# Optimization experiments

Hardware: AMD Instinct MI355X
Metric: run time of the kernel (lower is better)

Reference implementation:

```python
import jax, jax.numpy as jnp
import numpy as np

H = 8        # heads
DH = 64      # dim_head
K = 16       # num_neighbors
EMB = 512    # emb_dim
INNER = H * DH
AINNER = 4 * DH  # per-head attn_mlp hidden width
POSH = 64


def setup_inputs() -> dict:
    key = jax.random.key(0)
    ks = jax.random.split(key, 20)
    bs, n = 2, 1024
    rn = lambda k, s, sc=1.0: jax.random.normal(k, s, jnp.float32) * sc
    return {
        "query": rn(ks[0], (bs, n, EMB)),
        "key_in": rn(ks[1], (bs, n, EMB)),
        "value": rn(ks[2], (bs, n, EMB)),
        "canonical": rn(ks[3], (bs, n, 3)),
        "w_q": rn(ks[4], (EMB, INNER), EMB ** -0.5),
        "w_k": rn(ks[5], (EMB, INNER), EMB ** -0.5),
        "w_v": rn(ks[6], (EMB, INNER), EMB ** -0.5),
        "w_out": rn(ks[7], (INNER, EMB), INNER ** -0.5),
        "b_out": rn(ks[8], (EMB,), 0.02),
        "pos_w1": rn(ks[9], (3, POSH), 3 ** -0.5),
        "pos_b1": rn(ks[10], (POSH,), 0.02),
        "pos_w2": rn(ks[11], (POSH, INNER), POSH ** -0.5),
        "pos_b2": rn(ks[12], (INNER,), 0.02),
        "aw1": rn(ks[13], (H, AINNER, DH), DH ** -0.5),   # grouped conv1 weight per head: (out=4*DH, in=DH)
        "ab1": rn(ks[14], (H, AINNER), 0.02),
        "aw2": rn(ks[15], (H, DH, AINNER), AINNER ** -0.5),  # grouped conv2: (out=DH, in=4*DH)
        "ab2": rn(ks[16], (H, DH), 0.02),
    }


def reference(query, key_in, value, canonical, w_q, w_k, w_v, w_out, b_out,
              pos_w1, pos_b1, pos_w2, pos_b2, aw1, ab1, aw2, ab2):
    bs, n, _ = query.shape
    # projections, then b n (h d) -> b h n d
    to_heads = lambda t: t.reshape(bs, n, H, DH).transpose(0, 2, 1, 3)
    q = to_heads(query @ w_q)
    k = to_heads(key_in @ w_k)
    v = to_heads(value @ w_v)

    # KNN on canonical coords: (b,n,n) squared distances, k smallest (includes self)
    d2 = jnp.sum((canonical[:, :, None, :] - canonical[:, None, :, :]) ** 2, axis=-1)
    _, nbr = jax.lax.top_k(-d2, K)                       # (b,n,K)
    idx = (nbr + (jnp.arange(bs) * n)[:, None, None]).reshape(-1)  # flat rows into bs*n

    # relative position embedding
    pos_nn = canonical.reshape(bs * n, 3)[idx].reshape(bs, n, K, 3)
    rel = pos_nn - canonical[:, :, None, :]
    rpe = jax.nn.relu(rel @ pos_w1 + pos_b1) @ pos_w2 + pos_b2        # (b,n,K,inner)
    rpe = rpe.reshape(bs, n, K, H, DH).transpose(0, 3, 1, 2, 4)       # (b,h,i,j,d)

    # faithful replication of the original view(bs*n,-1)[idx] gathers on (b,h,n,d) tensors
    gather = lambda t: t.reshape(bs * n, -1)[idx].reshape(bs, H, n, K, DH)
    qg, kg, vg = gather(q), gather(k), gather(v)
    vg = vg + rpe
    x = (qg - kg) + rpe                                  # (b,h,i,j,d)

    # grouped 1x1 conv attn_mlp == per-head MLP over d
    hdn = jax.nn.relu(jnp.einsum('bhijd,hed->bhije', x, aw1) + ab1[None, :, None, None, :])
    sim = jnp.einsum('bhije,hde->bhijd', hdn, aw2) + ab2[None, :, None, None, :]

    attn = jax.nn.softmax(sim, axis=3)                   # softmax over neighbors j
    norm = jnp.sqrt(jnp.sum(attn * attn, axis=2, keepdims=True))  # F.normalize over i
    attn = attn / jnp.maximum(norm, 1e-12)

    agg = jnp.einsum('bhijd,bhijd->bhid', attn, vg)      # (b,h,i,d)
    agg = agg.transpose(0, 2, 1, 3).reshape(bs, n, INNER)
    return agg @ w_out + b_out
```

## Files before the change

kernel.cpp:

```cpp
#include <hip/hip_runtime.h>


#define BS 2
#define NPT 1024
#define HH 8
#define DH 64
#define KNN 16
#define EMB 512
#define INNER 512
#define AINNER 256
#define POSH 64

typedef unsigned short u16;
typedef unsigned int u32;
typedef __attribute__((ext_vector_type(8))) short bf16x8;
typedef __attribute__((ext_vector_type(4))) float f32x4;

__device__ __forceinline__ float bf2f(u16 b) { union { u32 u; float f; } v; v.u = ((u32)b) << 16; return v.f; }
__device__ __forceinline__ u16 f2bf_rne(float f) {
    u32 x = __float_as_uint(f);
    u32 r = x + 0x7fffu + ((x >> 16) & 1u);
    return (u16)(r >> 16);
}
__device__ __forceinline__ void split2(float f, u16& hi, u16& lo) {
    u32 bits = __float_as_uint(f);
    hi = (u16)(bits >> 16);
    float resid = f - __uint_as_float(bits & 0xffff0000u);
    lo = (u16)(__float_as_uint(resid) >> 16);
}
__device__ __forceinline__ void split4(float4 f, ushort4& h, ushort4& l) {
    split2(f.x, h.x, l.x); split2(f.y, h.y, l.y);
    split2(f.z, h.z, l.z); split2(f.w, h.w, l.w);
}

__global__ __launch_bounds__(256) void k_preT(const float* __restrict__ aw1,
                                              const float* __restrict__ aw2,
                                              const float* __restrict__ pw2,
                                              const float* __restrict__ wq,
                                              const float* __restrict__ wk,
                                              const float* __restrict__ wv,
                                              const float* __restrict__ wout,
                                              u16* __restrict__ w1hi, u16* __restrict__ w2hi,
                                              u16* __restrict__ rw2hi,
                                              u16* __restrict__ o0h, u16* __restrict__ o0l,
                                              u16* __restrict__ o1h, u16* __restrict__ o1l,
                                              u16* __restrict__ o2h, u16* __restrict__ o2l,
                                              u16* __restrict__ o3h, u16* __restrict__ o3l)
{
    __shared__ float S[64][65];
    const int bx = blockIdx.x, t = threadIdx.x;
    if (bx < 1152) {
        int idx = bx * 256 + t;
        if (idx < 131072) {
            w1hi[idx] = f2bf_rne(aw1[idx]);
        } else if (idx < 262144) {
            int k2 = idx - 131072;
            w2hi[k2] = f2bf_rne(aw2[k2]);
        } else {
            int k2 = idx - 262144;
            int p = k2 & 63; int hd = k2 >> 6;
            int h = hd >> 6; int d = hd & 63;
            rw2hi[k2] = f2bf_rne(pw2[(size_t)p * INNER + h * DH + d]);
        }
        return;
    }
    const int v0 = bx - 1152;
    const int e0 = (v0 & 7) * 64, c0 = ((v0 >> 3) & 7) * 64, z = v0 >> 6;
    const float* src; u16* dh; u16* dl;
    switch (z) {
        case 0:  src = wq;   dh = o0h; dl = o0l; break;
        case 1:  src = wk;   dh = o1h; dl = o1l; break;
        case 2:  src = wv;   dh = o2h; dl = o2l; break;
        default: src = wout; dh = o3h; dl = o3l; break;
    }
    #pragma unroll
    for (int s = 0; s < 16; ++s) {
        int v = s * 256 + t; int r = v >> 6, c = v & 63;
        S[r][c] = src[(size_t)(e0 + r) * 512 + c0 + c];
    }
    __syncthreads();
    #pragma unroll
    for (int s = 0; s < 16; ++s) {
        int v = s * 256 + t; int c = v >> 6, e = v & 63;
        u16 hi, lo; split2(S[e][c], hi, lo);
        size_t off = (size_t)(c0 + c) * 512 + e0 + e;
        dh[off] = hi; dl[off] = lo;
    }
}

__global__ __launch_bounds__(256) void k_projM(const float* __restrict__ qf,
                                               const float* __restrict__ kf,
                                               const float* __restrict__ vf,
                                               const u16* __restrict__ wqh, const u16* __restrict__ wql,
                                               const u16* __restrict__ wkh, const u16* __restrict__ wkl,
                                               const u16* __restrict__ wvh, const u16* __restrict__ wvl,
                                               float* __restrict__ Dws, float* __restrict__ Vws)
{
    __shared__ u16 S[12][64 * 40];
    const int t = threadIdx.x, l = t & 63, w = t >> 6;
    const int lm = l & 15, lg = (l >> 4) * 8;
    const int g0 = blockIdx.x * 64, c0 = blockIdx.y * 64;
    const int sr = t >> 2, sc = (t & 3) * 8;

    f32x4 accD[4] = {{0,0,0,0},{0,0,0,0},{0,0,0,0},{0,0,0,0}};
    f32x4 accV[4] = {{0,0,0,0},{0,0,0,0},{0,0,0,0},{0,0,0,0}};

    for (int ks = 0; ks < 16; ++ks) {
        const int k0 = ks * 32;
        if (ks) __syncthreads();
        #pragma unroll
        for (int m = 0; m < 3; ++m) {
            const float* sp = (m == 0 ? qf : (m == 1 ? kf : vf))
                              + (size_t)(g0 + sr) * 512 + k0 + sc;
            float4 f0 = *(const float4*)sp;
            float4 f1 = *(const float4*)(sp + 4);
            if (m == 1) {
                f0.x = -f0.x; f0.y = -f0.y; f0.z = -f0.z; f0.w = -f0.w;
                f1.x = -f1.x; f1.y = -f1.y; f1.z = -f1.z; f1.w = -f1.w;
            }
            ushort4 h0, l0, h1, l1;
            split4(f0, h0, l0); split4(f1, h1, l1);
            *(ushort4*)&S[2*m  ][sr * 40 + sc]     = h0;
            *(ushort4*)&S[2*m  ][sr * 40 + sc + 4] = h1;
            *(ushort4*)&S[2*m+1][sr * 40 + sc]     = l0;
            *(ushort4*)&S[2*m+1][sr * 40 + sc + 4] = l1;
        }
        #define STG(p, base) \
            *(uint4*)&S[p][sr * 40 + sc] = *(const uint4*)&(base)[(size_t)(c0 + sr) * 512 + k0 + sc];
        STG(6, wqh) STG(7, wql) STG(8, wkh) STG(9, wkl) STG(10, wvh) STG(11, wvl)
        #undef STG
        __syncthreads();

        const int ao = (w * 16 + lm) * 40 + lg;
        bf16x8 aqh = *(const bf16x8*)&S[0][ao];
        bf16x8 aql = *(const bf16x8*)&S[1][ao];
        bf16x8 akh = *(const bf16x8*)&S[2][ao];
        bf16x8 akl = *(const bf16x8*)&S[3][ao];
        bf16x8 avh = *(const bf16x8*)&S[4][ao];
        bf16x8 avl = *(const bf16x8*)&S[5][ao];
        #pragma unroll
        for (int ct = 0; ct < 4; ++ct) {
            const int bo = (ct * 16 + lm) * 40 + lg;
            bf16x8 bqh = *(const bf16x8*)&S[6][bo];
            bf16x8 bql = *(const bf16x8*)&S[7][bo];
            bf16x8 bkh = *(const bf16x8*)&S[8][bo];
            bf16x8 bkl = *(const bf16x8*)&S[9][bo];
            bf16x8 bvh = *(const bf16x8*)&S[10][bo];
            bf16x8 bvl = *(const bf16x8*)&S[11][bo];
            accD[ct] = __builtin_amdgcn_mfma_f32_16x16x32_bf16(aqh, bqh, accD[ct], 0, 0, 0);
            accD[ct] = __builtin_amdgcn_mfma_f32_16x16x32_bf16(aql, bqh, accD[ct], 0, 0, 0);
            accD[ct] = __builtin_amdgcn_mfma_f32_16x16x32_bf16(aqh, bql, accD[ct], 0, 0, 0);
            accD[ct] = __builtin_amdgcn_mfma_f32_16x16x32_bf16(akh, bkh, accD[ct], 0, 0, 0);
            accD[ct] = __builtin_amdgcn_mfma_f32_16x16x32_bf16(akl, bkh, accD[ct], 0, 0, 0);
            accD[ct] = __builtin_amdgcn_mfma_f32_16x16x32_bf16(akh, bkl, accD[ct], 0, 0, 0);
            accV[ct] = __builtin_amdgcn_mfma_f32_16x16x32_bf16(avh, bvh, accV[ct], 0, 0, 0);
            accV[ct] = __builtin_amdgcn_mfma_f32_16x16x32_bf16(avl, bvh, accV[ct], 0, 0, 0);
            accV[ct] = __builtin_amdgcn_mfma_f32_16x16x32_bf16(avh, bvl, accV[ct], 0, 0, 0);
        }
    }

    const int b = blockIdx.x >> 4;
    const int h = blockIdx.y;
    #pragma unroll
    for (int ct = 0; ct < 4; ++ct) {
        #pragma unroll
        for (int r = 0; r < 4; ++r) {
            int g = g0 + w * 16 + (l >> 4) * 4 + r;
            int i = g & 1023;
            size_t off = (((size_t)(b * HH + h)) * NPT + i) * DH + ct * 16 + lm;
            Dws[off] = accD[ct][r];
            Vws[off] = accV[ct][r];
        }
    }
}

__global__ __launch_bounds__(256) void k_knn(const float* __restrict__ canonical,
                                             const float* __restrict__ pw1,
                                             const float* __restrict__ pb1,
                                             int* __restrict__ nbr,
                                             u16* __restrict__ h1g)
{
    const int t = threadIdx.x, l = t & 63, w = t >> 6;
    const int i = blockIdx.x * 4 + w;
    const int b = blockIdx.y;
    const float* cb = canonical + (size_t)b * NPT * 3;
    const float qx = cb[i*3+0], qy = cb[i*3+1], qz = cb[i*3+2];
    float d2v[16];
    #pragma unroll
    for (int k = 0; k < 16; ++k) {
        int j = l * 16 + k;
        float dx = __fsub_rn(cb[j*3+0], qx);
        float dy = __fsub_rn(cb[j*3+1], qy);
        float dz = __fsub_rn(cb[j*3+2], qz);
        d2v[k] = __fadd_rn(__fadd_rn(__fmul_rn(dx,dx), __fmul_rn(dy,dy)), __fmul_rn(dz,dz));
    }
    unsigned alive = 0xFFFFu;
    int js[16];
    int* out = nbr + ((size_t)b * NPT + i) * KNN;
    #pragma unroll
    for (int sel = 0; sel < KNN; ++sel) {
        float bv = __builtin_inff(); int bk = 16;
        #pragma unroll
        for (int k = 0; k < 16; ++k) {
            float v = ((alive >> k) & 1u) ? d2v[k] : __builtin_inff();
            if (v < bv) { bv = v; bk = k; }
        }
        int bj = l * 16 + bk;
        #pragma unroll
        for (int m = 32; m >= 1; m >>= 1) {
            float ov = __shfl_xor(bv, m, 64);
            int   oj = __shfl_xor(bj, m, 64);
            if (ov < bv || (ov == bv && oj < bj)) { bv = ov; bj = oj; }
        }
        if (l == 0) out[sel] = bj;
        js[sel] = bj;
        if ((bj >> 4) == l) alive &= ~(1u << (bj & 15));
    }
    const float pw10 = pw1[l], pw11 = pw1[64 + l], pw12 = pw1[128 + l], pb1v = pb1[l];
    u16* hrow = h1g + (((size_t)b * NPT + i) * KNN) * 64 + l;
    #pragma unroll
    for (int j = 0; j < KNN; ++j) {
        int nv = js[j];
        float rx = cb[nv*3+0] - qx;
        float ry = cb[nv*3+1] - qy;
        float rz = cb[nv*3+2] - qz;
        float a = pb1v;
        a = fmaf(rx, pw10, a);
        a = fmaf(ry, pw11, a);
        a = fmaf(rz, pw12, a);
        hrow[j * 64] = f2bf_rne(fmaxf(a, 0.0f));
    }
}

__global__ __launch_bounds__(256, 3) void k_attn(const float* __restrict__ Dws,
                                              const float* __restrict__ Vws,
                                              const int* __restrict__ nbr,
                                              const float* __restrict__ pb2,
                                              const float* __restrict__ ab1,
                                              const float* __restrict__ ab2,
                                              const u16* __restrict__ w1hi,
                                              const u16* __restrict__ w2hi,
                                              const u16* __restrict__ rw2hi,
                                              const u16* __restrict__ h1g,
                                              u16* __restrict__ vvb,
                                              u16* __restrict__ attnb,
                                              float* __restrict__ npart2)
{
    const int it = blockIdx.x, h = blockIdx.y, b = blockIdx.z, t = threadIdx.x;
    const int l = t & 63, w = t >> 6;
    const int lm = l & 15, lg = (l >> 4) * 8;
    const int dd = w * 16 + lm;

    __shared__ u16 Xs[2][16 * 72];
    __shared__ u16 Hs[2][16 * 264];
    __shared__ u16 rw2s[64 * 72];
    __shared__ int nbrrow[KNN];

    bf16x8 w1f[8], w2f[8];
    float b1v[4];
    #pragma unroll
    for (int q = 0; q < 4; ++q) {
        int e = (w * 4 + q) * 16 + lm;
        b1v[q] = ab1[h * AINNER + e];
        #pragma unroll
        for (int kc = 0; kc < 2; ++kc)
            w1f[q*2+kc] = *(const bf16x8*)&w1hi[((size_t)(h * AINNER + e)) * DH + kc * 32 + lg];
    }
    const float b2v  = ab2[h * DH + dd];
    const float pb2v = pb2[h * DH + dd];
    #pragma unroll
    for (int kc = 0; kc < 8; ++kc)
        w2f[kc] = *(const bf16x8*)&w2hi[((size_t)(h * DH + dd)) * AINNER + kc * 32 + lg];

    for (int v = t; v < 64 * 64; v += 256) {
        int d = v >> 6, p = v & 63;
        rw2s[d * 72 + p] = rw2hi[(h * DH + d) * POSH + p];
    }
    if (t < KNN) nbrrow[t] = nbr[((size_t)b * NPT + h * 128 + it) * KNN + t];
    __syncthreads();

    float dvp[2][4], vwp[2][4];
    bf16x8 h1f[2][2];
    auto gather = [&](int pp) {
        #pragma unroll
        for (int u = 0; u < 2; ++u) {
            const int ti = 2 * pp + u;
            const int i = it * 8 + ti;
            #pragma unroll
            for (int r = 0; r < 4; ++r) {
                int j = (l >> 4) * 4 + r;
                int nv = nbrrow[2 * ti + (j >> 3)];
                size_t off = (((size_t)b * HH + (nv >> 7)) * NPT + (nv & 127) * 8 + (j & 7)) * DH + dd;
                dvp[u][r] = Dws[off];
                vwp[u][r] = Vws[off];
            }
            const u16* hb = h1g + (((size_t)b * NPT + i) * KNN + lm) * 64;
            h1f[u][0] = *(const bf16x8*)&hb[lg];
            h1f[u][1] = *(const bf16x8*)&hb[32 + lg];
        }
    };
    gather(0);

    float npacc[4] = {0.f, 0.f, 0.f, 0.f};

    for (int p = 0; p < 4; ++p) {
        #pragma unroll
        for (int u = 0; u < 2; ++u) {
            const int i = it * 8 + 2 * p + u;
            f32x4 racc = {0.f, 0.f, 0.f, 0.f};
            #pragma unroll
            for (int kc = 0; kc < 2; ++kc) {
                bf16x8 rb = *(const bf16x8*)&rw2s[dd * 72 + kc * 32 + lg];
                racc = __builtin_amdgcn_mfma_f32_16x16x32_bf16(h1f[u][kc], rb, racc, 0, 0, 0);
            }
            u16* vvrow = vvb + (((size_t)(b * HH + h) * NPT + i) * KNN) * DH + dd;
            #pragma unroll
            for (int r = 0; r < 4; ++r) {
                int j = (l >> 4) * 4 + r;
                float rp = racc[r] + pb2v;
                Xs[u][j * 72 + dd] = f2bf_rne(dvp[u][r] + rp);
                vvrow[j * DH] = f2bf_rne(vwp[u][r] + rp);
            }
        }
        if (p < 3) gather(p + 1);
        __syncthreads();
        #pragma unroll
        for (int u = 0; u < 2; ++u) {
            f32x4 acc1[4] = {{0,0,0,0},{0,0,0,0},{0,0,0,0},{0,0,0,0}};
            #pragma unroll
            for (int kc = 0; kc < 2; ++kc) {
                bf16x8 ah = *(const bf16x8*)&Xs[u][lm * 72 + kc * 32 + lg];
                #pragma unroll
                for (int q = 0; q < 4; ++q)
                    acc1[q] = __builtin_amdgcn_mfma_f32_16x16x32_bf16(ah, w1f[q*2+kc], acc1[q], 0, 0, 0);
            }
            #pragma unroll
            for (int q = 0; q < 4; ++q) {
                int ee = (w * 4 + q) * 16 + lm;
                #pragma unroll
                for (int r = 0; r < 4; ++r) {
                    int jj = (l >> 4) * 4 + r;
                    Hs[u][jj * 264 + ee] = f2bf_rne(fmaxf(acc1[q][r] + b1v[q], 0.0f));
                }
            }
        }
        __syncthreads();
        #pragma unroll
        for (int u = 0; u < 2; ++u) {
            const int i = it * 8 + 2 * p + u;
            f32x4 acc2[4] = {{0,0,0,0},{0,0,0,0},{0,0,0,0},{0,0,0,0}};
            #pragma unroll
            for (int kc = 0; kc < 8; ++kc) {
                bf16x8 ah = *(const bf16x8*)&Hs[u][lm * 264 + kc * 32 + lg];
                acc2[kc & 3] = __builtin_amdgcn_mfma_f32_16x16x32_bf16(ah, w2f[kc], acc2[kc & 3], 0, 0, 0);
            }
            float sim[4];
            #pragma unroll
            for (int r = 0; r < 4; ++r)
                sim[r] = ((acc2[0][r] + acc2[1][r]) + (acc2[2][r] + acc2[3][r])) + b2v;
            float m = fmaxf(fmaxf(sim[0], sim[1]), fmaxf(sim[2], sim[3]));
            m = fmaxf(m, __shfl_xor(m, 16, 64));
            m = fmaxf(m, __shfl_xor(m, 32, 64));
            float ex[4], s = 0.0f;
            #pragma unroll
            for (int r = 0; r < 4; ++r) { ex[r] = __expf(sim[r] - m); s += ex[r]; }
            s += __shfl_xor(s, 16, 64);
            s += __shfl_xor(s, 32, 64);
            float inv = 1.0f / s;
            u16* ao = attnb + (((size_t)(b * HH + h) * NPT + i) * KNN) * DH + dd;
            #pragma unroll
            for (int r = 0; r < 4; ++r) {
                u16 abf16 = f2bf_rne(ex[r] * inv);
                ao[((l >> 4) * 4 + r) * DH] = abf16;
                float abf = bf2f(abf16);
                npacc[r] = fmaf(abf, abf, npacc[r]);
            }
        }
    }

    float* np = npart2 + ((size_t)((b * HH + h) * 128 + it)) * 1024 + ((l >> 4) * 4) * 64 + dd;
    #pragma unroll
    for (int r = 0; r < 4; ++r) np[r * 64] = npacc[r];
}

__global__ __launch_bounds__(256) void k_normR(const float* __restrict__ npart2, float* __restrict__ nrm)
{
    __shared__ float red[256];
    const int vout = blockIdx.x * 64 + (threadIdx.x & 63);
    const int chunk = threadIdx.x >> 6;
    const int bh = vout >> 10, jd = vout & 1023;
    const float* src = npart2 + (size_t)bh * 131072 + jd + (size_t)chunk * 32768;
    float s = 0.0f;
    #pragma unroll 4
    for (int k = 0; k < 32; ++k) s += src[k * 1024];
    red[threadIdx.x] = s;
    __syncthreads();
    if (chunk == 0) {
        float tot = (red[threadIdx.x] + red[threadIdx.x + 64])
                  + (red[threadIdx.x + 128] + red[threadIdx.x + 192]);
        nrm[vout] = sqrtf(tot);
    }
}

__global__ __launch_bounds__(256) void k_agg(const u16* __restrict__ attnb,
                                             const float* __restrict__ nrm,
                                             const u16* __restrict__ vvb,
                                             u16* __restrict__ agghi,
                                             u16* __restrict__ agglo)
{
    const int it = blockIdx.x, h = blockIdx.y, b = blockIdx.z, t = threadIdx.x;
    const int l = t & 63, w = t >> 6;
    const int i = it * 4 + w;
    __shared__ float rn[KNN * DH];
    for (int v = t; v < KNN * DH; v += 256)
        rn[v] = 1.0f / fmaxf(nrm[(size_t)(b * HH + h) * 1024 + v], 1e-12f);
    __syncthreads();
    const size_t row = ((size_t)(b * HH + h) * NPT + i) * (KNN * DH);
    bf16x8 a0 = *(const bf16x8*)&attnb[row + l * 8];
    bf16x8 a1 = *(const bf16x8*)&attnb[row + 512 + l * 8];
    bf16x8 q0 = *(const bf16x8*)&vvb[row + l * 8];
    bf16x8 q1 = *(const bf16x8*)&vvb[row + 512 + l * 8];
    const int dbase = (l & 7) * 8;
    float4 ra = *(const float4*)&rn[(l >> 3) * 64 + dbase];
    float4 rb = *(const float4*)&rn[(l >> 3) * 64 + dbase + 4];
    float4 rc = *(const float4*)&rn[(8 + (l >> 3)) * 64 + dbase];
    float4 rd = *(const float4*)&rn[(8 + (l >> 3)) * 64 + dbase + 4];
    const float r0[8] = {ra.x, ra.y, ra.z, ra.w, rb.x, rb.y, rb.z, rb.w};
    const float r1[8] = {rc.x, rc.y, rc.z, rc.w, rd.x, rd.y, rd.z, rd.w};
    float acc[8];
    #pragma unroll
    for (int e = 0; e < 8; ++e)
        acc[e] = bf2f((u16)a0[e]) * r0[e] * bf2f((u16)q0[e])
               + bf2f((u16)a1[e]) * r1[e] * bf2f((u16)q1[e]);
    #pragma unroll
    for (int mask = 8; mask <= 32; mask <<= 1)
        #pragma unroll
        for (int e = 0; e < 8; ++e)
            acc[e] += __shfl_xor(acc[e], mask, 64);
    if (l < 8) {
        size_t off = ((size_t)b * NPT + i) * INNER + h * DH + l * 8;
        ushort4 h0, l0, h1, l1;
        split2(acc[0], h0.x, l0.x); split2(acc[1], h0.y, l0.y);
        split2(acc[2], h0.z, l0.z); split2(acc[3], h0.w, l0.w);
        split2(acc[4], h1.x, l1.x); split2(acc[5], h1.y, l1.y);
        split2(acc[6], h1.z, l1.z); split2(acc[7], h1.w, l1.w);
        *(ushort4*)&agghi[off]     = h0;
        *(ushort4*)&agghi[off + 4] = h1;
        *(ushort4*)&agglo[off]     = l0;
        *(ushort4*)&agglo[off + 4] = l1;
    }
}

__global__ __launch_bounds__(256) void k_outM(const u16* __restrict__ agghi, const u16* __restrict__ agglo,
                                              const u16* __restrict__ wth, const u16* __restrict__ wtl,
                                              const float* __restrict__ bout,
                                              float* __restrict__ outp)
{
    __shared__ u16 S[4][64 * 40];
    const int t = threadIdx.x, l = t & 63, w = t >> 6;
    const int lm = l & 15, lg = (l >> 4) * 8;
    const int g0 = blockIdx.x * 64, c0 = blockIdx.y * 64;
    const int sr = t >> 2, sc = (t & 3) * 8;

    f32x4 acc[4] = {{0,0,0,0},{0,0,0,0},{0,0,0,0},{0,0,0,0}};
    float bv4[4];
    #pragma unroll
    for (int ct = 0; ct < 4; ++ct) bv4[ct] = bout[c0 + ct * 16 + lm];

    for (int ks = 0; ks < 16; ++ks) {
        const int k0 = ks * 32;
        if (ks) __syncthreads();
        *(uint4*)&S[0][sr * 40 + sc] = *(const uint4*)&agghi[(size_t)(g0 + sr) * 512 + k0 + sc];
        *(uint4*)&S[1][sr * 40 + sc] = *(const uint4*)&agglo[(size_t)(g0 + sr) * 512 + k0 + sc];
        *(uint4*)&S[2][sr * 40 + sc] = *(const uint4*)&wth[(size_t)(c0 + sr) * 512 + k0 + sc];
        *(uint4*)&S[3][sr * 40 + sc] = *(const uint4*)&wtl[(size_t)(c0 + sr) * 512 + k0 + sc];
        __syncthreads();

        const int ao = (w * 16 + lm) * 40 + lg;
        bf16x8 ah = *(const bf16x8*)&S[0][ao];
        bf16x8 al = *(const bf16x8*)&S[1][ao];
        #pragma unroll
        for (int ct = 0; ct < 4; ++ct) {
            const int bo = (ct * 16 + lm) * 40 + lg;
            bf16x8 bh = *(const bf16x8*)&S[2][bo];
            bf16x8 bl = *(const bf16x8*)&S[3][bo];
            acc[ct] = __builtin_amdgcn_mfma_f32_16x16x32_bf16(ah, bh, acc[ct], 0, 0, 0);
            acc[ct] = __builtin_amdgcn_mfma_f32_16x16x32_bf16(al, bh, acc[ct], 0, 0, 0);
            acc[ct] = __builtin_amdgcn_mfma_f32_16x16x32_bf16(ah, bl, acc[ct], 0, 0, 0);
        }
    }
    #pragma unroll
    for (int ct = 0; ct < 4; ++ct) {
        #pragma unroll
        for (int r = 0; r < 4; ++r) {
            int g = g0 + w * 16 + (l >> 4) * 4 + r;
            outp[(size_t)g * 512 + c0 + ct * 16 + lm] = acc[ct][r] + bv4[ct];
        }
    }
}

extern "C" void kernel_launch(void* const* d_in, const int* in_sizes, int n_in,
                              void* d_out, int out_size, void* d_ws, size_t ws_size,
                              hipStream_t stream) {
    const float* query     = (const float*)d_in[0];
    const float* key_in    = (const float*)d_in[1];
    const float* value     = (const float*)d_in[2];
    const float* canonical = (const float*)d_in[3];
    const float* wq   = (const float*)d_in[4];
    const float* wk   = (const float*)d_in[5];
    const float* wv   = (const float*)d_in[6];
    const float* wout = (const float*)d_in[7];
    const float* bout = (const float*)d_in[8];
    const float* pw1  = (const float*)d_in[9];
    const float* pb1  = (const float*)d_in[10];
    const float* pw2  = (const float*)d_in[11];
    const float* pb2  = (const float*)d_in[12];
    const float* aw1  = (const float*)d_in[13];
    const float* ab1  = (const float*)d_in[14];
    const float* aw2  = (const float*)d_in[15];
    const float* ab2  = (const float*)d_in[16];

    float* ws    = (float*)d_ws;
    float* Dws   = ws;
    float* Vws   = ws + 1048576;
    float* aggp  = ws + 2097152;
    float* nrm   = ws + 3162112;
    int*   nbr   = (int*)(ws + 3293184);
    float* attnR = ws + 3325952;

    u16* agghi = (u16*)aggp;
    u16* agglo = agghi + 1048576;

    u16* attnb = (u16*)attnR;
    u16* pl   = (u16*)(attnR + 8388608);
    u16* wqTh = pl;                u16* wqTl = pl + 262144;
    u16* wkTh = pl + 524288;       u16* wkTl = pl + 786432;
    u16* wvTh = pl + 1048576;      u16* wvTl = pl + 1310720;
    float* npart2 = attnR + 12582912;
    u16* h1g = (u16*)(attnR + 14680064);

    u16* u16b  = (u16*)(ws + 20103168);
    u16* w1hi  = u16b;
    u16* w2hi  = u16b + 262144;
    u16* rw2hi = u16b + 524288;
    u16* vvb   = u16b + 589824;
    u16* wouTh = u16b + 17367040;
    u16* wouTl = u16b + 17629184;

    k_preT<<<1408, 256, 0, stream>>>(aw1, aw2, pw2, wq, wk, wv, wout,
                                     w1hi, w2hi, rw2hi,
                                     wqTh, wqTl, wkTh, wkTl, wvTh, wvTl, wouTh, wouTl);
    k_knn<<<dim3(256, BS), 256, 0, stream>>>(canonical, pw1, pb1, nbr, h1g);
    k_projM<<<dim3(32, 8), 256, 0, stream>>>(query, key_in, value,
                                             wqTh, wqTl, wkTh, wkTl, wvTh, wvTl, Dws, Vws);
    k_attn<<<dim3(128, HH, BS), 256, 0, stream>>>(Dws, Vws, nbr, pb2, ab1, ab2,
                                                  w1hi, w2hi, rw2hi, h1g, vvb, attnb, npart2);
    k_normR<<<256, 256, 0, stream>>>(npart2, nrm);
    k_agg<<<dim3(256, HH, BS), 256, 0, stream>>>(attnb, nrm, vvb, agghi, agglo);
    k_outM<<<dim3(32, 8), 256, 0, stream>>>(agghi, agglo, wouTh, wouTl, bout, (float*)d_out);
}
```

Measured before the change: 148.4 us.

## Fuse attn*value product into attention kernel and register-prefetch GEMM tiles

The attention kernel now multiplies the softmax weights by the value-plus-position term in registers and writes a single bf16 product buffer, instead of writing separate attention and value buffers. The aggregation kernel then reads only that one buffer and scales it by the per-(i,d) inverse norm, which halves the large intermediate traffic. The two projection GEMM kernels also prefetch the next K-slice into registers while the current tile is computed, to hide global load latency. This costs extra registers, which may lower occupancy, and it changes rounding because the product is rounded to bf16 once rather than each factor separately.

Measured after the change: 169.7 us. 14.4% more time.

```diff
diff --git a/kernel.cpp b/kernel.cpp
--- a/kernel.cpp
+++ b/kernel.cpp
@@ -105,15 +105,31 @@
     f32x4 accD[4] = {{0,0,0,0},{0,0,0,0},{0,0,0,0},{0,0,0,0}};
     f32x4 accV[4] = {{0,0,0,0},{0,0,0,0},{0,0,0,0},{0,0,0,0}};
 
-    for (int ks = 0; ks < 16; ++ks) {
+    float4 fA[3][2];
+    uint4  wB[6];
+    auto ldregs = [&](int ks) {
         const int k0 = ks * 32;
-        if (ks) __syncthreads();
         #pragma unroll
         for (int m = 0; m < 3; ++m) {
             const float* sp = (m == 0 ? qf : (m == 1 ? kf : vf))
                               + (size_t)(g0 + sr) * 512 + k0 + sc;
-            float4 f0 = *(const float4*)sp;
-            float4 f1 = *(const float4*)(sp + 4);
+            fA[m][0] = *(const float4*)sp;
+            fA[m][1] = *(const float4*)(sp + 4);
+        }
+        wB[0] = *(const uint4*)&wqh[(size_t)(c0 + sr) * 512 + k0 + sc];
+        wB[1] = *(const uint4*)&wql[(size_t)(c0 + sr) * 512 + k0 + sc];
+        wB[2] = *(const uint4*)&wkh[(size_t)(c0 + sr) * 512 + k0 + sc];
+        wB[3] = *(const uint4*)&wkl[(size_t)(c0 + sr) * 512 + k0 + sc];
+        wB[4] = *(const uint4*)&wvh[(size_t)(c0 + sr) * 512 + k0 + sc];
+        wB[5] = *(const uint4*)&wvl[(size_t)(c0 + sr) * 512 + k0 + sc];
+    };
+    ldregs(0);
+
+    for (int ks = 0; ks < 16; ++ks) {
+        if (ks) __syncthreads();
+        #pragma unroll
+        for (int m = 0; m < 3; ++m) {
+            float4 f0 = fA[m][0], f1 = fA[m][1];
             if (m == 1) {
                 f0.x = -f0.x; f0.y = -f0.y; f0.z = -f0.z; f0.w = -f0.w;
                 f1.x = -f1.x; f1.y = -f1.y; f1.z = -f1.z; f1.w = -f1.w;
@@ -125,11 +141,11 @@
             *(ushort4*)&S[2*m+1][sr * 40 + sc]     = l0;
             *(ushort4*)&S[2*m+1][sr * 40 + sc + 4] = l1;
         }
-        #define STG(p, base) \
-            *(uint4*)&S[p][sr * 40 + sc] = *(const uint4*)&(base)[(size_t)(c0 + sr) * 512 + k0 + sc];
-        STG(6, wqh) STG(7, wql) STG(8, wkh) STG(9, wkl) STG(10, wvh) STG(11, wvl)
-        #undef STG
+        #pragma unroll
+        for (int p = 0; p < 6; ++p)
+            *(uint4*)&S[6 + p][sr * 40 + sc] = wB[p];
         __syncthreads();
+        if (ks < 15) ldregs(ks + 1);
 
         const int ao = (w * 16 + lm) * 40 + lg;
         bf16x8 aqh = *(const bf16x8*)&S[0][ao];
@@ -242,8 +258,7 @@
                                               const u16* __restrict__ w2hi,
                                               const u16* __restrict__ rw2hi,
                                               const u16* __restrict__ h1g,
-                                              u16* __restrict__ vvb,
-                                              u16* __restrict__ attnb,
+                                              u16* __restrict__ prodb,
                                               float* __restrict__ npart2)
 {
     const int it = blockIdx.x, h = blockIdx.y, b = blockIdx.z, t = threadIdx.x;
@@ -302,24 +317,23 @@
     gather(0);
 
     float npacc[4] = {0.f, 0.f, 0.f, 0.f};
+    float vvreg[2][4];
 
     for (int p = 0; p < 4; ++p) {
         #pragma unroll
         for (int u = 0; u < 2; ++u) {
-            const int i = it * 8 + 2 * p + u;
             f32x4 racc = {0.f, 0.f, 0.f, 0.f};
             #pragma unroll
             for (int kc = 0; kc < 2; ++kc) {
                 bf16x8 rb = *(const bf16x8*)&rw2s[dd * 72 + kc * 32 + lg];
                 racc = __builtin_amdgcn_mfma_f32_16x16x32_bf16(h1f[u][kc], rb, racc, 0, 0, 0);
             }
-            u16* vvrow = vvb + (((size_t)(b * HH + h) * NPT + i) * KNN) * DH + dd;
             #pragma unroll
             for (int r = 0; r < 4; ++r) {
                 int j = (l >> 4) * 4 + r;
                 float rp = racc[r] + pb2v;
                 Xs[u][j * 72 + dd] = f2bf_rne(dvp[u][r] + rp);
-                vvrow[j * DH] = f2bf_rne(vwp[u][r] + rp);
+                vvreg[u][r] = vwp[u][r] + rp;
             }
         }
         if (p < 3) gather(p + 1);
@@ -367,13 +381,12 @@
             s += __shfl_xor(s, 16, 64);
             s += __shfl_xor(s, 32, 64);
             float inv = 1.0f / s;
-            u16* ao = attnb + (((size_t)(b * HH + h) * NPT + i) * KNN) * DH + dd;
+            u16* po = prodb + (((size_t)(b * HH + h) * NPT + i) * KNN) * DH + dd;
             #pragma unroll
             for (int r = 0; r < 4; ++r) {
-                u16 abf16 = f2bf_rne(ex[r] * inv);
-                ao[((l >> 4) * 4 + r) * DH] = abf16;
-                float abf = bf2f(abf16);
-                npacc[r] = fmaf(abf, abf, npacc[r]);
+                float af = ex[r] * inv;
+                po[((l >> 4) * 4 + r) * DH] = f2bf_rne(af * vvreg[u][r]);
+                npacc[r] = fmaf(af, af, npacc[r]);
             }
         }
     }
@@ -402,9 +415,8 @@
     }
 }
 
-__global__ __launch_bounds__(256) void k_agg(const u16* __restrict__ attnb,
+__global__ __launch_bounds__(256) void k_agg(const u16* __restrict__ prodb,
                                              const float* __restrict__ nrm,
-                                             const u16* __restrict__ vvb,
                                              u16* __restrict__ agghi,
                                              u16* __restrict__ agglo)
 {
@@ -416,10 +428,8 @@
         rn[v] = 1.0f / fmaxf(nrm[(size_t)(b * HH + h) * 1024 + v], 1e-12f);
     __syncthreads();
     const size_t row = ((size_t)(b * HH + h) * NPT + i) * (KNN * DH);
-    bf16x8 a0 = *(const bf16x8*)&attnb[row + l * 8];
-    bf16x8 a1 = *(const bf16x8*)&attnb[row + 512 + l * 8];
-    bf16x8 q0 = *(const bf16x8*)&vvb[row + l * 8];
-    bf16x8 q1 = *(const bf16x8*)&vvb[row + 512 + l * 8];
+    bf16x8 p0 = *(const bf16x8*)&prodb[row + l * 8];
+    bf16x8 p1 = *(const bf16x8*)&prodb[row + 512 + l * 8];
     const int dbase = (l & 7) * 8;
     float4 ra = *(const float4*)&rn[(l >> 3) * 64 + dbase];
     float4 rb = *(const float4*)&rn[(l >> 3) * 64 + dbase + 4];
@@ -430,8 +440,7 @@
     float acc[8];
     #pragma unroll
     for (int e = 0; e < 8; ++e)
-        acc[e] = bf2f((u16)a0[e]) * r0[e] * bf2f((u16)q0[e])
-               + bf2f((u16)a1[e]) * r1[e] * bf2f((u16)q1[e]);
+        acc[e] = bf2f((u16)p0[e]) * r0[e] + bf2f((u16)p1[e]) * r1[e];
     #pragma unroll
     for (int mask = 8; mask <= 32; mask <<= 1)
         #pragma unroll
@@ -467,14 +476,23 @@
     #pragma unroll
     for (int ct = 0; ct < 4; ++ct) bv4[ct] = bout[c0 + ct * 16 + lm];
 
+    uint4 rA[4];
+    auto ldregs = [&](int ks) {
+        const int k0 = ks * 32;
+        rA[0] = *(const uint4*)&agghi[(size_t)(g0 + sr) * 512 + k0 + sc];
+        rA[1] = *(const uint4*)&agglo[(size_t)(g0 + sr) * 512 + k0 + sc];
+        rA[2] = *(const uint4*)&wth[(size_t)(c0 + sr) * 512 + k0 + sc];
+        rA[3] = *(const uint4*)&wtl[(size_t)(c0 + sr) * 512 + k0 + sc];
+    };
+    ldregs(0);
+
     for (int ks = 0; ks < 16; ++ks) {
-        const int k0 = ks * 32;
         if (ks) __syncthreads();
-        *(uint4*)&S[0][sr * 40 + sc] = *(const uint4*)&agghi[(size_t)(g0 + sr) * 512 + k0 + sc];
-        *(uint4*)&S[1][sr * 40 + sc] = *(const uint4*)&agglo[(size_t)(g0 + sr) * 512 + k0 + sc];
-        *(uint4*)&S[2][sr * 40 + sc] = *(const uint4*)&wth[(size_t)(c0 + sr) * 512 + k0 + sc];
-        *(uint4*)&S[3][sr * 40 + sc] = *(const uint4*)&wtl[(size_t)(c0 + sr) * 512 + k0 + sc];
+        #pragma unroll
+        for (int p = 0; p < 4; ++p)
+            *(uint4*)&S[p][sr * 40 + sc] = rA[p];
         __syncthreads();
+        if (ks < 15) ldregs(ks + 1);
 
         const int ao = (w * 16 + lm) * 40 + lg;
         bf16x8 ah = *(const bf16x8*)&S[0][ao];
@@ -531,7 +549,7 @@
     u16* agghi = (u16*)aggp;
     u16* agglo = agghi + 1048576;
 
-    u16* attnb = (u16*)attnR;
+    u16* prodb = (u16*)attnR;
     u16* pl   = (u16*)(attnR + 8388608);
     u16* wqTh = pl;                u16* wqTl = pl + 262144;
     u16* wkTh = pl + 524288;       u16* wkTl = pl + 786432;
@@ -543,7 +561,6 @@
     u16* w1hi  = u16b;
     u16* w2hi  = u16b + 262144;
     u16* rw2hi = u16b + 524288;
-    u16* vvb   = u16b + 589824;
     u16* wouTh = u16b + 17367040;
     u16* wouTl = u16b + 17629184;
 
@@ -554,8 +571,8 @@
     k_projM<<<dim3(32, 8), 256, 0, stream>>>(query, key_in, value,
                                              wqTh, wqTl, wkTh, wkTl, wvTh, wvTl, Dws, Vws);
     k_attn<<<dim3(128, HH, BS), 256, 0, stream>>>(Dws, Vws, nbr, pb2, ab1, ab2,
-                                                  w1hi, w2hi, rw2hi, h1g, vvb, attnb, npart2);
+                                                  w1hi, w2hi, rw2hi, h1g, prodb, npart2);
     k_normR<<<256, 256, 0, stream>>>(npart2, nrm);
-    k_agg<<<dim3(256, HH, BS), 256, 0, stream>>>(attnb, nrm, vvb, agghi, agglo);
+    k_agg<<<dim3(256, HH, BS), 256, 0, stream>>>(prodb, nrm, agghi, agglo);
     k_outM<<<dim3(32, 8), 256, 0, stream>>>(agghi, agglo, wouTh, wouTl, bout, (float*)d_out);
 }
```
